# Optimization experiments

Hardware: AMD Instinct MI355X
Metric: run time of the kernel (lower is better)

Reference implementation:

```python
import jax, jax.numpy as jnp
import numpy as np

NZ = 128
N_GEN = 8
BATCH = 2048
SLOPE = 0.2


def _convt(x, w, b, stride, pad):
    # PyTorch ConvTranspose2d(weight [Cin,Cout,kH,kW], stride, padding p)
    # == conv with lhs_dilation=stride, padding=k-1-p, spatially-flipped
    # kernel with in/out channels swapped.
    k = jnp.flip(w, axis=(2, 3)).transpose(2, 3, 0, 1)  # [kH,kW,Cin,Cout]
    y = jax.lax.conv_general_dilated(
        x, k, window_strides=(1, 1), padding=[(pad, pad), (pad, pad)],
        lhs_dilation=(stride, stride),
        dimension_numbers=('NCHW', 'HWIO', 'NCHW'))
    return y + b[None, :, None, None]


def setup_inputs() -> dict:
    key = jax.random.key(0)
    ks = jax.random.split(key, 12)
    s = 0.05
    return {
        'z': jax.random.normal(ks[0], (BATCH, NZ), jnp.float32),
        'g_idx': jax.random.randint(ks[1], (BATCH,), 0, N_GEN),
        'W1': jax.random.normal(ks[2], (N_GEN, NZ, 256), jnp.float32) * s,
        'b1': jax.random.normal(ks[3], (N_GEN, 256), jnp.float32) * s,
        'W2': jax.random.normal(ks[4], (N_GEN, 256, 1568), jnp.float32) * s,
        'b2': jax.random.normal(ks[5], (N_GEN, 1568), jnp.float32) * s,
        'cw1': jax.random.normal(ks[6], (N_GEN, 32, 16, 4, 4), jnp.float32) * s,
        'cb1': jax.random.normal(ks[7], (N_GEN, 16), jnp.float32) * s,
        'cw2': jax.random.normal(ks[8], (N_GEN, 16, 8, 4, 4), jnp.float32) * s,
        'cb2': jax.random.normal(ks[9], (N_GEN, 8), jnp.float32) * s,
        'cw3': jax.random.normal(ks[10], (N_GEN, 8, 1, 3, 3), jnp.float32) * s,
        'cb3': jax.random.normal(ks[11], (N_GEN, 1), jnp.float32) * s,
    }


def _single_gen(params, z):
    W1, b1, W2, b2, cw1, cb1, cw2, cb2, cw3, cb3 = params
    lrelu = lambda x: jax.nn.leaky_relu(x, SLOPE)
    h = lrelu(z @ W1 + b1)                 # [B,256]
    h = lrelu(h @ W2 + b2)                 # [B,1568]
    h = h.reshape(-1, 32, 7, 7)
    h = lrelu(_convt(h, cw1, cb1, 2, 2))   # [B,16,14,14]
    h = lrelu(_convt(h, cw2, cb2, 2, 2))   # [B,8,28,28]
    return jnp.tanh(_convt(h, cw3, cb3, 1, 1))  # [B,1,28,28]


def reference(z, g_idx, W1, b1, W2, b2, cw1, cb1, cw2, cb2, cw3, cb3):
    params = (W1, b1, W2, b2, cw1, cb1, cw2, cb2, cw3, cb3)
    # Compute every generator on the full batch (faithful to the torch loop),
    # vmapped over the generator axis: images [G,B,1,28,28].
    images = jax.vmap(_single_gen, in_axes=((0,) * 10, None))(params, z)
    # Per-sample gather: keep generator g_idx[b] for each sample b.
    return images[g_idx, jnp.arange(z.shape[0])]
```

## Files before the change

### kernel.cpp

```cpp
#include <hip/hip_runtime.h>
#include <cstdint>
#include <cstddef>

#define BATCH 2048
#define NZ 128
#define NGEN 8
#define GRPS 32
#define MAXG 72
#define NCT 13
#define H2_ELEMS 1792
#define WS_H1_OFF 16384
#define WS_H2_OFF (16384 + MAXG * 8192 * 4)
#define WS_W2T_OFF (WS_H2_OFF + BATCH * H2_ELEMS * 2)
#define W2T_GSTRIDE (1568 * 256)
#define NB_W2T (NGEN * 49)
#define NB_PREP (NB_W2T + MAXG * 4)
#define WS_WPK1_OFF (WS_W2T_OFF + NGEN * W2T_GSTRIDE * 2)
#define WS_WPK2_OFF (WS_WPK1_OFF + NGEN * 4096 * 4)
#define WS_WPK3_OFF (WS_WPK2_OFF + NGEN * 1024 * 4)

typedef unsigned int u32;
typedef unsigned short u16;
typedef _Float16 f16x8 __attribute__((ext_vector_type(8)));
typedef _Float16 f16x4 __attribute__((ext_vector_type(4)));
typedef _Float16 f16x2 __attribute__((ext_vector_type(2)));
typedef float f32x4 __attribute__((ext_vector_type(4)));

__device__ __forceinline__ float lrelu(float x) { return fmaxf(x, 0.2f * x); }
__device__ __forceinline__ u16 f16b(float f) {
    _Float16 h = (_Float16)f;
    return __builtin_bit_cast(u16, h);
}
__device__ __forceinline__ u32 pk2(float a, float b) {
    f16x2 v; v[0] = (_Float16)a; v[1] = (_Float16)b;
    return __builtin_bit_cast(u32, v);
}
__device__ __forceinline__ float dot2(u32 a, u32 b, float c) {
#if __has_builtin(__builtin_amdgcn_fdot2)
    return __builtin_amdgcn_fdot2(__builtin_bit_cast(f16x2, a),
                                  __builtin_bit_cast(f16x2, b), c, false);
#else
    float d;
    asm("v_dot2_f32_f16 %0, %1, %2, %3" : "=v"(d) : "v"(a), "v"(b), "v"(c));
    return d;
#endif
}
__device__ __forceinline__ float fast_tanh(float x) {
    x = fminf(fmaxf(x, -9.f), 9.f);
    const float e = __expf(2.f * x);
    return (e - 1.f) / (e + 1.f);
}

__global__ void bin_kernel(const int* __restrict__ g_idx, int* __restrict__ wsi) {
    __shared__ int cnt[NGEN];
    __shared__ int pbase[NGEN + 1];
    __shared__ u16 rank[BATCH];
    const int tid = threadIdx.x;
    if (tid < NGEN) cnt[tid] = 0;
    __syncthreads();
    for (int b = tid; b < BATCH; b += 256) {
        int g = g_idx[b];
        rank[b] = (u16)atomicAdd(&cnt[g], 1);
    }
    __syncthreads();
    if (tid == 0) {
        int acc = 0;
        for (int g = 0; g < NGEN; ++g) {
            pbase[g] = acc;
            acc += ((cnt[g] + GRPS - 1) / GRPS) * GRPS;
        }
        pbase[NGEN] = acc;
        wsi[0] = acc;
    }
    __syncthreads();
    const int total = pbase[NGEN];
    for (int i = tid; i < total; i += 256) wsi[16 + i] = -1;
    __syncthreads();
    for (int b = tid; b < BATCH; b += 256) {
        int g = g_idx[b];
        wsi[16 + pbase[g] + (int)rank[b]] = b;
    }
}

__global__ __launch_bounds__(256) void prep_kernel(
    const float* __restrict__ z, const int* __restrict__ g_idx,
    const float* __restrict__ W1, const float* __restrict__ b1,
    const float* __restrict__ W2, const int* __restrict__ wsi,
    float* __restrict__ h1g, _Float16* __restrict__ W2T,
    const float* __restrict__ cw1, const float* __restrict__ cw2,
    const float* __restrict__ cw3,
    u32* __restrict__ wpk1, u32* __restrict__ wpk2, u32* __restrict__ wpk3)
{
    __shared__ _Float16 t[32][264];
    __shared__ float zst[NZ][12];
    __shared__ int sb[8];
    __shared__ int sG;

    const int tid = threadIdx.x;
    const int bx = blockIdx.x;

    if (bx >= NB_PREP) {
        const int g = bx - NB_PREP;
        const float* c1p = cw1 + g * 8192;
        u32* o1 = wpk1 + g * 4096;
        for (int i = tid; i < 4096; i += 256) {
            const int cip = i >> 8, a = (i >> 6) & 3, co = (i >> 2) & 15, c = i & 3;
            const float* s = c1p + cip * 512 + co * 16 + a * 4 + c;
            o1[i] = pk2(s[0], s[256]);
        }
        const float* c2p = cw2 + g * 2048;
        u32* o2 = wpk2 + g * 1024;
        for (int i = tid; i < 1024; i += 256) {
            const int cip = i >> 7, a = (i >> 5) & 3, co = (i >> 2) & 7, c = i & 3;
            const float* s = c2p + cip * 256 + co * 16 + a * 4 + c;
            o2[i] = pk2(s[0], s[128]);
        }
        if (tid < 36) {
            const int cip = tid / 9, r = tid % 9;
            const float* s = cw3 + g * 72 + cip * 18 + r;
            wpk3[g * 36 + tid] = pk2(s[0], s[9]);
        }
        return;
    }

    if (bx < NB_W2T) {
        const int g = bx / 49;
        const int n0 = (bx % 49) * 32;
        const float* src = W2 + (size_t)g * 256 * 1568;
        const int nl = tid & 31, kh = tid >> 5;
        #pragma unroll 8
        for (int p = 0; p < 32; ++p) {
            const int k = p * 8 + kh;
            t[nl][k] = (_Float16)src[(size_t)k * 1568 + n0 + nl];
        }
        __syncthreads();
        _Float16* dst = W2T + (size_t)g * W2T_GSTRIDE + (size_t)n0 * 256;
        const int n = tid >> 3, k0 = (tid & 7) * 32;
        #pragma unroll
        for (int j = 0; j < 4; ++j)
            *(uint4*)(dst + (size_t)n * 256 + k0 + 8 * j) = *(const uint4*)&t[n][k0 + 8 * j];
        return;
    }

    const int bx2 = bx - NB_W2T;
    const int grp = bx2 >> 2;
    const int s0 = (bx2 & 3) * 8;
    if (grp * GRPS >= wsi[0]) return;

    if (tid == 0) sG = g_idx[wsi[16 + grp * GRPS]];
    if (tid < 8) sb[tid] = wsi[16 + grp * GRPS + s0 + tid];
    __syncthreads();
    const float* W1g = W1 + sG * (NZ * 256);
    const float* b1g = b1 + sG * 256;

    {
        const int s = tid >> 5, f = tid & 31;
        float4 v = make_float4(0.f, 0.f, 0.f, 0.f);
        if (sb[s] >= 0) v = *(const float4*)(z + (size_t)sb[s] * NZ + 4 * f);
        zst[4 * f + 0][s] = v.x; zst[4 * f + 1][s] = v.y;
        zst[4 * f + 2][s] = v.z; zst[4 * f + 3][s] = v.w;
    }
    __syncthreads();

    const int c = tid;
    float acc[8];
    #pragma unroll
    for (int s = 0; s < 8; ++s) acc[s] = 0.f;
    const float* wp = W1g + c;
    #pragma unroll 4
    for (int k = 0; k < NZ; ++k) {
        const float w = wp[k * 256];
        float av[8];
        *(float4*)&av[0] = *(const float4*)&zst[k][0];
        *(float4*)&av[4] = *(const float4*)&zst[k][4];
        #pragma unroll
        for (int s = 0; s < 8; ++s) acc[s] += av[s] * w;
    }
    const float bv = b1g[c];
    float* hp = h1g + (size_t)grp * 8192 + (size_t)s0 * 256 + c;
    #pragma unroll
    for (int s = 0; s < 8; ++s) hp[s * 256] = lrelu(acc[s] + bv);
}

__global__ __launch_bounds__(256) void fc2_kernel(
    const int* __restrict__ g_idx,
    const _Float16* __restrict__ W2T, const float* __restrict__ b2,
    const int* __restrict__ wsi, const float* __restrict__ h1g,
    u16* __restrict__ h2g)
{
    __shared__ _Float16 afrag[2 * 2 * 8 * 64 * 8];
    __shared__ int sb[GRPS];
    __shared__ int sG;

    const int tid = threadIdx.x;
    const int grp = blockIdx.x / NCT;
    const int tile = blockIdx.x % NCT;
    if (grp * GRPS >= wsi[0]) return;

    if (tid == 0) sG = g_idx[wsi[16 + grp * GRPS]];
    if (tid < GRPS) sb[tid] = wsi[16 + grp * GRPS + tid];
    __syncthreads();
    const _Float16* W2Tg = W2T + (size_t)sG * W2T_GSTRIDE;
    const float* b2g = b2 + sG * 1568;

    {
        const float4* h1p4 = (const float4*)(h1g + (size_t)grp * 8192);
        #pragma unroll
        for (int i = 0; i < 8; ++i) {
            const int u = tid + 256 * i;
            const int j4 = u & 1;
            const int lane = (u >> 1) & 63;
            const int kq = (u >> 7) & 7;
            const int mt = (u >> 10) & 1;
            const int s = mt * 16 + (lane & 15);
            const float4 v = h1p4[s * 64 + kq * 8 + ((lane >> 4) << 1) + j4];
            const float vv[4] = {v.x, v.y, v.z, v.w};
            f16x4 hi, lo;
            #pragma unroll
            for (int e = 0; e < 4; ++e) {
                hi[e] = (_Float16)vv[e];
                lo[e] = (_Float16)(vv[e] - (float)hi[e]);
            }
            const int bh = (((mt * 2 + 0) * 8 + kq) * 64 + lane) * 8 + 4 * j4;
            const int bl = (((mt * 2 + 1) * 8 + kq) * 64 + lane) * 8 + 4 * j4;
            *(f16x4*)&afrag[bh] = hi;
            *(f16x4*)&afrag[bl] = lo;
        }
    }
    __syncthreads();

    const int wave = tid >> 6;
    const int lane = tid & 63;
    const int q = lane >> 4;
    const int nl = lane & 15;
    const int nb0 = tile * 128 + 2 * wave * 16;
    if (nb0 >= 1568) return;

    #pragma unroll
    for (int nt = 0; nt < 2; ++nt) {
        const int nb = nb0 + nt * 16;
        if (nb >= 1568) break;
        const int n = nb + nl;
        const _Float16* bp = W2Tg + (size_t)n * 256 + q * 8;
        f32x4 accA = {0.f, 0.f, 0.f, 0.f}, accB = accA;
        #pragma unroll
        for (int kq = 0; kq < 8; ++kq) {
            const f16x8 b = *(const f16x8*)(bp + kq * 32);
            const f16x8 a0h = *(const f16x8*)&afrag[((0 * 8 + kq) * 64 + lane) * 8];
            const f16x8 a0l = *(const f16x8*)&afrag[((1 * 8 + kq) * 64 + lane) * 8];
            const f16x8 a1h = *(const f16x8*)&afrag[((2 * 8 + kq) * 64 + lane) * 8];
            const f16x8 a1l = *(const f16x8*)&afrag[((3 * 8 + kq) * 64 + lane) * 8];
            accA = __builtin_amdgcn_mfma_f32_16x16x32_f16(a0h, b, accA, 0, 0, 0);
            accA = __builtin_amdgcn_mfma_f32_16x16x32_f16(a0l, b, accA, 0, 0, 0);
            accB = __builtin_amdgcn_mfma_f32_16x16x32_f16(a1h, b, accB, 0, 0, 0);
            accB = __builtin_amdgcn_mfma_f32_16x16x32_f16(a1l, b, accB, 0, 0, 0);
        }
        const float bias = b2g[n];
        const int ci = n / 49, rm = n % 49;
        const int off = ci * 56 + (rm / 7) * 8 + (rm % 7);
        #pragma unroll
        for (int mt = 0; mt < 2; ++mt) {
            const f32x4 a = (mt == 0) ? accA : accB;
            #pragma unroll
            for (int reg = 0; reg < 4; ++reg) {
                const int s = mt * 16 + q * 4 + reg;
                const int bb = sb[s];
                if (bb >= 0)
                    h2g[(size_t)bb * H2_ELEMS + off] = f16b(lrelu(a[reg] + bias));
            }
        }
    }
}

template <int H>
__device__ __forceinline__ void conv2p_half(
    const u32 (*c1s)[14][20], u16* dst,
    const u32* __restrict__ w2g, const float bv, const int co, const int y)
{
    float acc[14];
    #pragma unroll
    for (int xx = 0; xx < 14; ++xx) acc[xx] = bv;
    const int a0 = (y + 1) & 1;
    for (int aa = 0; aa < 2; ++aa) {
        const int a = a0 + 2 * aa;
        const int iy = (y + 1 - a) >> 1;
        if ((unsigned)iy < 14u) {
            #pragma unroll 2
            for (int cip = 0; cip < 8; ++cip) {
                u32 rr[10];
                if (H == 0) {
                    *(uint4*)&rr[0] = *(const uint4*)&c1s[cip][iy][0];
                    *(uint4*)&rr[4] = *(const uint4*)&c1s[cip][iy][4];
                } else {
                    *(uint4*)&rr[0] = *(const uint4*)&c1s[cip][iy][4];
                    *(uint4*)&rr[4] = *(const uint4*)&c1s[cip][iy][8];
                    *(uint2*)&rr[8] = *(const uint2*)&c1s[cip][iy][12];
                }
                const uint4 wq = *(const uint4*)(w2g + ((cip * 4 + a) * 8 + co) * 4);
                const u32 wv[4] = {wq.x, wq.y, wq.z, wq.w};
                #pragma unroll
                for (int xx = 0; xx < 14; ++xx) {
                    const int x = 14 * H + xx;
                    const int c0v = (x + 1) & 1;
                    const int ix0 = (x + 1 - c0v) >> 1;
                    const int li = ix0 - 4 * H;
                    if (ix0 < 14) acc[xx] = dot2(rr[li],     wv[c0v],     acc[xx]);
                    if (ix0 >= 1) acc[xx] = dot2(rr[li - 1], wv[c0v + 2], acc[xx]);
                }
            }
        }
    }
    #pragma unroll
    for (int xx = 0; xx < 14; ++xx) dst[2 * (14 * H + xx)] = f16b(lrelu(acc[xx]));
}

__global__ __launch_bounds__(256, 6) void conv_kernel(
    const int* __restrict__ g_idx,
    const u32* __restrict__ wpk1, const float* __restrict__ cb1,
    const u32* __restrict__ wpk2, const float* __restrict__ cb2,
    const u32* __restrict__ wpk3, const float* __restrict__ cb3,
    const u16* __restrict__ h2g, float* __restrict__ out)
{
    __shared__ __align__(16) char smem[8960 + 14784];
    u32 (*c1s)[14][20] = (u32 (*)[14][20])smem;
    u32 (*h2s)[7][8]   = (u32 (*)[7][8])(smem + 8960);
    u32 (*c2s)[28][33] = (u32 (*)[28][33])(smem + 8960);
    __shared__ u32 w3s[36];

    const int tid = threadIdx.x;
    const int b = blockIdx.x;
    const int g = g_idx[b];
    const u32* w1g = wpk1 + g * 4096;
    const u32* w2g = wpk2 + g * 1024;
    const float* cb1g = cb1 + g * 16;
    const float* cb2g = cb2 + g * 8;
    const float  cb3v = cb3[g];

    if (tid < 224) {
        const uint4 qv = ((const uint4*)(h2g + (size_t)b * H2_ELEMS))[tid];
        const int ci = tid / 7, yq = tid % 7;
        u16* dst = (u16*)&h2s[ci >> 1][yq][0] + (ci & 1);
        const u32 w[4] = {qv.x, qv.y, qv.z, qv.w};
        #pragma unroll
        for (int j = 0; j < 4; ++j) {
            dst[4 * j]     = (u16)(w[j] & 0xffffu);
            dst[4 * j + 2] = (u16)(w[j] >> 16);
        }
    }
    if (tid < 36) w3s[tid] = wpk3[g * 36 + tid];
    __syncthreads();

    if (tid < 224) {
        const int co = tid / 14, y = tid % 14;
        const float bv = cb1g[co];
        float acc[14];
        #pragma unroll
        for (int x = 0; x < 14; ++x) acc[x] = bv;
        const int a0 = (y + 1) & 1;
        for (int aa = 0; aa < 2; ++aa) {
            const int a = a0 + 2 * aa;
            const int iy = (y + 1 - a) >> 1;
            if ((unsigned)iy < 7u) {
                #pragma unroll 2
                for (int cip = 0; cip < 16; ++cip) {
                    u32 rr[8];
                    *(uint4*)&rr[0] = *(const uint4*)&h2s[cip][iy][0];
                    *(uint4*)&rr[4] = *(const uint4*)&h2s[cip][iy][4];
                    const uint4 wq = *(const uint4*)(w1g + ((cip * 4 + a) * 16 + co) * 4);
                    const u32 wv[4] = {wq.x, wq.y, wq.z, wq.w};
                    #pragma unroll
                    for (int x = 0; x < 14; ++x) {
                        const int c0v = (x + 1) & 1;
                        const int ix0 = (x + 1 - c0v) >> 1;
                        if (ix0 < 7)  acc[x] = dot2(rr[ix0],     wv[c0v],     acc[x]);
                        if (ix0 >= 1) acc[x] = dot2(rr[ix0 - 1], wv[c0v + 2], acc[x]);
                    }
                }
            }
        }
        u16* dst = (u16*)&c1s[co >> 1][y][0] + (co & 1);
        #pragma unroll
        for (int x = 0; x < 14; ++x) dst[2 * x] = f16b(lrelu(acc[x]));
    }
    __syncthreads();

    if (tid < 224) {
        const int co = tid / 28, y = tid % 28;
        const float bv = cb2g[co];
        u16* dst = (u16*)&c2s[co >> 1][y][0] + (co & 1);
        conv2p_half<0>(c1s, dst, w2g, bv, co, y);
        conv2p_half<1>(c1s, dst, w2g, bv, co, y);
    }
    __syncthreads();

    if (tid < 196) {
        const int y = tid / 7, qq = tid % 7;
        const int xb = qq * 4;
        float acc[4] = {cb3v, cb3v, cb3v, cb3v};
        #pragma unroll 2
        for (int cip = 0; cip < 4; ++cip) {
            u32 wp[9];
            #pragma unroll
            for (int j = 0; j < 9; ++j) wp[j] = w3s[cip * 9 + j];
            #pragma unroll
            for (int a = 0; a < 3; ++a) {
                const int iy = y + 1 - a;
                if ((unsigned)iy < 28u) {
                    u32 rr[6];
                    #pragma unroll
                    for (int j = 0; j < 6; ++j) {
                        const int ix = xb - 1 + j;
                        rr[j] = ((unsigned)ix < 28u) ? c2s[cip][iy][ix] : 0u;
                    }
                    #pragma unroll
                    for (int xx = 0; xx < 4; ++xx)
                        #pragma unroll
                        for (int c = 0; c < 3; ++c)
                            acc[xx] = dot2(rr[xx + 2 - c], wp[a * 3 + c], acc[xx]);
                }
            }
        }
        float* op = out + (size_t)b * 784 + y * 28 + xb;
        #pragma unroll
        for (int xx = 0; xx < 4; ++xx) op[xx] = fast_tanh(acc[xx]);
    }
}

extern "C" void kernel_launch(void* const* d_in, const int* in_sizes, int n_in,
                              void* d_out, int out_size, void* d_ws, size_t ws_size,
                              hipStream_t stream) {
    const float* z   = (const float*)d_in[0];
    const int*   gi  = (const int*)d_in[1];
    const float* W1  = (const float*)d_in[2];
    const float* b1  = (const float*)d_in[3];
    const float* W2  = (const float*)d_in[4];
    const float* b2  = (const float*)d_in[5];
    const float* cw1 = (const float*)d_in[6];
    const float* cb1 = (const float*)d_in[7];
    const float* cw2 = (const float*)d_in[8];
    const float* cb2 = (const float*)d_in[9];
    const float* cw3 = (const float*)d_in[10];
    const float* cb3 = (const float*)d_in[11];
    int*      wsi = (int*)d_ws;
    float*    h1g = (float*)((char*)d_ws + WS_H1_OFF);
    u16*      h2g = (u16*)((char*)d_ws + WS_H2_OFF);
    _Float16* w2t = (_Float16*)((char*)d_ws + WS_W2T_OFF);
    u32*      wpk1 = (u32*)((char*)d_ws + WS_WPK1_OFF);
    u32*      wpk2 = (u32*)((char*)d_ws + WS_WPK2_OFF);
    u32*      wpk3 = (u32*)((char*)d_ws + WS_WPK3_OFF);

    bin_kernel<<<1, 256, 0, stream>>>(gi, wsi);
    prep_kernel<<<NB_PREP + NGEN, 256, 0, stream>>>(z, gi, W1, b1, W2, wsi, h1g, w2t,
                                                    cw1, cw2, cw3, wpk1, wpk2, wpk3);
    fc2_kernel<<<MAXG * NCT, 256, 0, stream>>>(gi, w2t, b2, wsi, h1g, h2g);
    conv_kernel<<<BATCH, 256, 0, stream>>>(gi, wpk1, cb1, wpk2, cb2, wpk3, cb3,
                                           h2g, (float*)d_out);
}
```

Measured before the change: 166.5 us.

## Drop split-fp16 FC2 compensation, ballot-based binning, shrink conv smem

```diff
diff --git a/kernel.cpp b/kernel.cpp
--- a/kernel.cpp
+++ b/kernel.cpp
@@ -21,6 +21,7 @@
 
 typedef unsigned int u32;
 typedef unsigned short u16;
+typedef unsigned long long u64;
 typedef _Float16 f16x8 __attribute__((ext_vector_type(8)));
 typedef _Float16 f16x4 __attribute__((ext_vector_type(4)));
 typedef _Float16 f16x2 __attribute__((ext_vector_type(2)));
@@ -52,33 +53,51 @@
 }
 
 __global__ void bin_kernel(const int* __restrict__ g_idx, int* __restrict__ wsi) {
-    __shared__ int cnt[NGEN];
+    __shared__ int wcnt[4][NGEN];
+    __shared__ int wboff[4][NGEN];
     __shared__ int pbase[NGEN + 1];
     __shared__ u16 rank[BATCH];
     const int tid = threadIdx.x;
-    if (tid < NGEN) cnt[tid] = 0;
-    __syncthreads();
-    for (int b = tid; b < BATCH; b += 256) {
-        int g = g_idx[b];
-        rank[b] = (u16)atomicAdd(&cnt[g], 1);
+    const int w = tid >> 6, lane = tid & 63;
+    if (tid < 4 * NGEN) wcnt[tid >> 3][tid & 7] = 0;
+    __syncthreads();
+    const u64 lt = ((u64)1 << lane) - 1;
+    #pragma unroll
+    for (int r = 0; r < 8; ++r) {
+        const int b = r * 256 + tid;
+        const int gg = g_idx[b];
+        u64 m[NGEN];
+        #pragma unroll
+        for (int k = 0; k < NGEN; ++k) m[k] = __ballot(gg == k);
+        rank[b] = (u16)((int)__popcll(m[gg] & lt) + wcnt[w][gg]);
+        if (lane < NGEN) wcnt[w][lane] += (int)__popcll(m[lane]);
     }
     __syncthreads();
     if (tid == 0) {
         int acc = 0;
         for (int g = 0; g < NGEN; ++g) {
             pbase[g] = acc;
-            acc += ((cnt[g] + GRPS - 1) / GRPS) * GRPS;
+            const int tot = wcnt[0][g] + wcnt[1][g] + wcnt[2][g] + wcnt[3][g];
+            acc += ((tot + GRPS - 1) / GRPS) * GRPS;
         }
         pbase[NGEN] = acc;
         wsi[0] = acc;
     }
     __syncthreads();
+    if (tid < 32) {
+        const int ww = tid >> 3, g = tid & 7;
+        int off = pbase[g];
+        for (int w2 = 0; w2 < ww; ++w2) off += wcnt[w2][g];
+        wboff[ww][g] = off;
+    }
     const int total = pbase[NGEN];
     for (int i = tid; i < total; i += 256) wsi[16 + i] = -1;
     __syncthreads();
-    for (int b = tid; b < BATCH; b += 256) {
-        int g = g_idx[b];
-        wsi[16 + pbase[g] + (int)rank[b]] = b;
+    #pragma unroll
+    for (int r = 0; r < 8; ++r) {
+        const int b = r * 256 + tid;
+        const int gg = g_idx[b];
+        wsi[16 + wboff[w][gg] + (int)rank[b]] = b;
     }
 }
 
@@ -188,7 +207,7 @@
     const int* __restrict__ wsi, const float* __restrict__ h1g,
     u16* __restrict__ h2g)
 {
-    __shared__ _Float16 afrag[2 * 2 * 8 * 64 * 8];
+    __shared__ _Float16 afrag[2 * 8 * 64 * 8];
     __shared__ int sb[GRPS];
     __shared__ int sG;
 
@@ -209,22 +228,16 @@
         for (int i = 0; i < 8; ++i) {
             const int u = tid + 256 * i;
             const int j4 = u & 1;
-            const int lane = (u >> 1) & 63;
+            const int ln = (u >> 1) & 63;
             const int kq = (u >> 7) & 7;
             const int mt = (u >> 10) & 1;
-            const int s = mt * 16 + (lane & 15);
-            const float4 v = h1p4[s * 64 + kq * 8 + ((lane >> 4) << 1) + j4];
-            const float vv[4] = {v.x, v.y, v.z, v.w};
-            f16x4 hi, lo;
-            #pragma unroll
-            for (int e = 0; e < 4; ++e) {
-                hi[e] = (_Float16)vv[e];
-                lo[e] = (_Float16)(vv[e] - (float)hi[e]);
-            }
-            const int bh = (((mt * 2 + 0) * 8 + kq) * 64 + lane) * 8 + 4 * j4;
-            const int bl = (((mt * 2 + 1) * 8 + kq) * 64 + lane) * 8 + 4 * j4;
+            const int s = mt * 16 + (ln & 15);
+            const float4 v = h1p4[s * 64 + kq * 8 + ((ln >> 4) << 1) + j4];
+            f16x4 hi;
+            hi[0] = (_Float16)v.x; hi[1] = (_Float16)v.y;
+            hi[2] = (_Float16)v.z; hi[3] = (_Float16)v.w;
+            const int bh = ((mt * 8 + kq) * 64 + ln) * 8 + 4 * j4;
             *(f16x4*)&afrag[bh] = hi;
-            *(f16x4*)&afrag[bl] = lo;
         }
     }
     __syncthreads();
@@ -246,14 +259,10 @@
         #pragma unroll
         for (int kq = 0; kq < 8; ++kq) {
             const f16x8 b = *(const f16x8*)(bp + kq * 32);
-            const f16x8 a0h = *(const f16x8*)&afrag[((0 * 8 + kq) * 64 + lane) * 8];
-            const f16x8 a0l = *(const f16x8*)&afrag[((1 * 8 + kq) * 64 + lane) * 8];
-            const f16x8 a1h = *(const f16x8*)&afrag[((2 * 8 + kq) * 64 + lane) * 8];
-            const f16x8 a1l = *(const f16x8*)&afrag[((3 * 8 + kq) * 64 + lane) * 8];
-            accA = __builtin_amdgcn_mfma_f32_16x16x32_f16(a0h, b, accA, 0, 0, 0);
-            accA = __builtin_amdgcn_mfma_f32_16x16x32_f16(a0l, b, accA, 0, 0, 0);
-            accB = __builtin_amdgcn_mfma_f32_16x16x32_f16(a1h, b, accB, 0, 0, 0);
-            accB = __builtin_amdgcn_mfma_f32_16x16x32_f16(a1l, b, accB, 0, 0, 0);
+            const f16x8 a0 = *(const f16x8*)&afrag[((0 * 8 + kq) * 64 + lane) * 8];
+            const f16x8 a1 = *(const f16x8*)&afrag[((1 * 8 + kq) * 64 + lane) * 8];
+            accA = __builtin_amdgcn_mfma_f32_16x16x32_f16(a0, b, accA, 0, 0, 0);
+            accB = __builtin_amdgcn_mfma_f32_16x16x32_f16(a1, b, accB, 0, 0, 0);
         }
         const float bias = b2g[n];
         const int ci = n / 49, rm = n % 49;
@@ -314,17 +323,17 @@
     for (int xx = 0; xx < 14; ++xx) dst[2 * (14 * H + xx)] = f16b(lrelu(acc[xx]));
 }
 
-__global__ __launch_bounds__(256, 6) void conv_kernel(
+__global__ __launch_bounds__(256, 7) void conv_kernel(
     const int* __restrict__ g_idx,
     const u32* __restrict__ wpk1, const float* __restrict__ cb1,
     const u32* __restrict__ wpk2, const float* __restrict__ cb2,
     const u32* __restrict__ wpk3, const float* __restrict__ cb3,
     const u16* __restrict__ h2g, float* __restrict__ out)
 {
-    __shared__ __align__(16) char smem[8960 + 14784];
+    __shared__ __align__(16) char smem[8960 + 12992];
     u32 (*c1s)[14][20] = (u32 (*)[14][20])smem;
     u32 (*h2s)[7][8]   = (u32 (*)[7][8])(smem + 8960);
-    u32 (*c2s)[28][33] = (u32 (*)[28][33])(smem + 8960);
+    u32 (*c2s)[28][29] = (u32 (*)[28][29])(smem + 8960);
     __shared__ u32 w3s[36];
 
     const int tid = threadIdx.x;
```

New measurement: 166.4 us. Within noise of the previous version (-0.1%).
